# Kernel tuning notes

Measured on AMD Instinct MI355X. Metric: run time of the kernel, lower is better.

## Reference

```python
import jax, jax.numpy as jnp
import numpy as np

EPS = 1e-9


def _elementwise_ciou(b1, b2):
    # b1, b2: [..., 4] xyxy boxes. Direct O(N) CIoU (== diag of pairwise CIoU).
    x1a, y1a, x2a, y2a = b1[..., 0], b1[..., 1], b1[..., 2], b1[..., 3]
    x1b, y1b, x2b, y2b = b2[..., 0], b2[..., 1], b2[..., 2], b2[..., 3]

    iw = jnp.clip(jnp.minimum(x2a, x2b) - jnp.maximum(x1a, x1b), 0.0)
    ih = jnp.clip(jnp.minimum(y2a, y2b) - jnp.maximum(y1a, y1b), 0.0)
    inter = iw * ih
    area_a = (x2a - x1a) * (y2a - y1a)
    area_b = (x2b - x1b) * (y2b - y1b)
    union = area_a + area_b - inter
    iou = inter / (union + EPS)

    # enclosing box diagonal squared
    cw = jnp.maximum(x2a, x2b) - jnp.minimum(x1a, x1b)
    ch = jnp.maximum(y2a, y2b) - jnp.minimum(y1a, y1b)
    c2 = cw * cw + ch * ch + EPS

    # center distance squared
    dx = (x1b + x2b - x1a - x2a) * 0.5
    dy = (y1b + y2b - y1a - y2a) * 0.5
    rho2 = dx * dx + dy * dy

    # aspect-ratio consistency term
    wa, ha = x2a - x1a, y2a - y1a
    wb, hb = x2b - x1b, y2b - y1b
    v = (4.0 / (jnp.pi ** 2)) * jnp.square(
        jnp.arctan(wb / (hb + EPS)) - jnp.arctan(wa / (ha + EPS)))
    alpha = v / (1.0 - iou + v + EPS)
    return iou - rho2 / c2 - alpha * v


def _make_boxes(key, B, A):
    k1, k2 = jax.random.split(key)
    cxy = jax.random.uniform(k1, (B, A, 2), jnp.float32, 0.0, 1280.0)
    wh = jax.random.uniform(k2, (B, A, 2), jnp.float32, 4.0, 200.0)
    return jnp.concatenate([cxy - wh * 0.5, cxy + wh * 0.5], axis=-1)


def setup_inputs() -> dict:
    key = jax.random.key(0)
    B, A = 64, 33600
    k1, k2, k3, k4 = jax.random.split(key, 4)
    predicts_bbox = _make_boxes(k1, B, A)
    targets_bbox = _make_boxes(k2, B, A)
    valid_masks = jax.random.bernoulli(k3, 0.3, (B, A))
    box_norm = jax.random.uniform(k4, (B, A), jnp.float32) * valid_masks
    cls_norm = jnp.maximum(valid_masks.sum().astype(jnp.float32), 1.0)
    return {
        "predicts_bbox": predicts_bbox,
        "targets_bbox": targets_bbox,
        "valid_masks": valid_masks,
        "box_norm": box_norm,
        "cls_norm": cls_norm,
    }


def reference(predicts_bbox, targets_bbox, valid_masks, box_norm, cls_norm):
    m = valid_masks.astype(predicts_bbox.dtype)  # [B, A]
    iou = _elementwise_ciou(predicts_bbox, targets_bbox) * m
    loss_iou = ((1.0 - iou) * box_norm * m).sum() / cls_norm
    return loss_iou, iou
```

## Files before the change

kernel.cpp:

```cpp
#include <hip/hip_runtime.h>
#include <math.h>

#define EPSF 1e-9f

__global__ __launch_bounds__(256) void box_loss_kernel(
    const float4* __restrict__ pb, const float4* __restrict__ tb,
    const int*    __restrict__ mask, const float* __restrict__ bnorm,
    const float*  __restrict__ cls_norm, float* __restrict__ out, int n)
{
    const int stride = gridDim.x * blockDim.x;
    float acc = 0.0f;
    for (int i = blockIdx.x * blockDim.x + threadIdx.x; i < n; i += stride) {
        const float4 a = pb[i];
        const float4 b = tb[i];

        float iw = fminf(a.z, b.z) - fmaxf(a.x, b.x); iw = fmaxf(iw, 0.0f);
        float ih = fminf(a.w, b.w) - fmaxf(a.y, b.y); ih = fmaxf(ih, 0.0f);
        float inter = iw * ih;

        float wa = a.z - a.x, ha = a.w - a.y;
        float wb = b.z - b.x, hb = b.w - b.y;
        float uni = wa * ha + wb * hb - inter;
        float iou = inter / (uni + EPSF);

        float cw = fmaxf(a.z, b.z) - fminf(a.x, b.x);
        float ch = fmaxf(a.w, b.w) - fminf(a.y, b.y);
        float c2 = cw * cw + ch * ch + EPSF;

        float dx = (b.x + b.z - a.x - a.z) * 0.5f;
        float dy = (b.y + b.w - a.y - a.w) * 0.5f;
        float rho2 = dx * dx + dy * dy;

        float datan = atanf(wb / (hb + EPSF)) - atanf(wa / (ha + EPSF));
        const float c4pi2 = 4.0f / (float)(M_PI * M_PI);
        float v = c4pi2 * datan * datan;
        float alpha = v / (1.0f - iou + v + EPSF);

        float ciou = iou - rho2 / c2 - alpha * v;

        float m = (float)mask[i];
        float iou_m = ciou * m;
        out[1 + i] = iou_m;
        acc += (1.0f - iou_m) * bnorm[i] * m;
    }

    #pragma unroll
    for (int off = 32; off > 0; off >>= 1)
        acc += __shfl_down(acc, off, 64);

    __shared__ float lds[4];
    const int lane = threadIdx.x & 63;
    const int wid  = threadIdx.x >> 6;
    if (lane == 0) lds[wid] = acc;
    __syncthreads();
    if (threadIdx.x == 0) {
        float s = lds[0] + lds[1] + lds[2] + lds[3];
        atomicAdd(out, s / cls_norm[0]);
    }
}

extern "C" void kernel_launch(void* const* d_in, const int* in_sizes, int n_in,
                              void* d_out, int out_size, void* d_ws, size_t ws_size,
                              hipStream_t stream) {
    const float4* pb    = (const float4*)d_in[0];
    const float4* tb    = (const float4*)d_in[1];
    const int*    mask  = (const int*)  d_in[2];
    const float*  bnorm = (const float*)d_in[3];
    const float*  cls   = (const float*)d_in[4];
    float*        out   = (float*)d_out;
    const int n = in_sizes[2];

    hipMemsetAsync(d_out, 0, sizeof(float), stream);

    const int block = 256;
    const int grid  = 2048;
    box_loss_kernel<<<grid, block, 0, stream>>>(pb, tb, mask, bnorm, cls, out, n);
}
```

Baseline: 134.1 us.

## Replace atanf pair with single polynomial atan, use rcp, unroll loads

```diff
diff --git a/kernel.cpp b/kernel.cpp
--- a/kernel.cpp
+++ b/kernel.cpp
@@ -2,6 +2,55 @@
 #include <math.h>
 
 #define EPSF 1e-9f
+#define UNROLL 4
+
+__device__ __forceinline__ float fast_atan(float z) {
+    float az = fabsf(z);
+    float rz = __builtin_amdgcn_rcpf(az);
+    float t  = az > 1.0f ? rz : az;
+    float t2 = t * t;
+    float p = fmaf(t2, 0.0208351f, -0.0851330f);
+    p = fmaf(t2, p, 0.1801410f);
+    p = fmaf(t2, p, -0.3302995f);
+    p = fmaf(t2, p, 0.9998660f);
+    p = p * t;
+    float r = az > 1.0f ? 1.5707963f - p : p;
+    return z < 0.0f ? -r : r;
+}
+
+__device__ __forceinline__ float ciou_masked(float4 a, float4 b, float m,
+                                             float bn, float* acc) {
+    float iw = fminf(a.z, b.z) - fmaxf(a.x, b.x); iw = fmaxf(iw, 0.0f);
+    float ih = fminf(a.w, b.w) - fmaxf(a.y, b.y); ih = fmaxf(ih, 0.0f);
+    float inter = iw * ih;
+
+    float wa = a.z - a.x, ha = a.w - a.y;
+    float wb = b.z - b.x, hb = b.w - b.y;
+    float uni = wa * ha + wb * hb - inter;
+    float iou = inter * __builtin_amdgcn_rcpf(uni + EPSF);
+
+    float cw = fmaxf(a.z, b.z) - fminf(a.x, b.x);
+    float ch = fmaxf(a.w, b.w) - fminf(a.y, b.y);
+    float c2 = fmaf(cw, cw, fmaf(ch, ch, EPSF));
+
+    float dx = (b.x + b.z - a.x - a.z) * 0.5f;
+    float dy = (b.y + b.w - a.y - a.w) * 0.5f;
+    float rho2 = fmaf(dx, dx, dy * dy);
+
+    float hap = ha + EPSF, hbp = hb + EPSF;
+    float num = fmaf(wb, hap, -wa * hbp);
+    float den = fmaf(hap, hbp, wa * wb);
+    float datan = fast_atan(num * __builtin_amdgcn_rcpf(den));
+
+    const float c4pi2 = 0.40528473456f;
+    float v = c4pi2 * datan * datan;
+    float av = v * v * __builtin_amdgcn_rcpf(1.0f - iou + v + EPSF);
+
+    float ciou = iou - rho2 * __builtin_amdgcn_rcpf(c2) - av;
+    float iou_m = ciou * m;
+    *acc += (1.0f - iou_m) * bn * m;
+    return iou_m;
+}
 
 __global__ __launch_bounds__(256) void box_loss_kernel(
     const float4* __restrict__ pb, const float4* __restrict__ tb,
@@ -9,39 +58,25 @@
     const float*  __restrict__ cls_norm, float* __restrict__ out, int n)
 {
     const int stride = gridDim.x * blockDim.x;
+    const int tid = blockIdx.x * blockDim.x + threadIdx.x;
     float acc = 0.0f;
-    for (int i = blockIdx.x * blockDim.x + threadIdx.x; i < n; i += stride) {
-        const float4 a = pb[i];
-        const float4 b = tb[i];
 
-        float iw = fminf(a.z, b.z) - fmaxf(a.x, b.x); iw = fmaxf(iw, 0.0f);
-        float ih = fminf(a.w, b.w) - fmaxf(a.y, b.y); ih = fmaxf(ih, 0.0f);
-        float inter = iw * ih;
-
-        float wa = a.z - a.x, ha = a.w - a.y;
-        float wb = b.z - b.x, hb = b.w - b.y;
-        float uni = wa * ha + wb * hb - inter;
-        float iou = inter / (uni + EPSF);
-
-        float cw = fmaxf(a.z, b.z) - fminf(a.x, b.x);
-        float ch = fmaxf(a.w, b.w) - fminf(a.y, b.y);
-        float c2 = cw * cw + ch * ch + EPSF;
-
-        float dx = (b.x + b.z - a.x - a.z) * 0.5f;
-        float dy = (b.y + b.w - a.y - a.w) * 0.5f;
-        float rho2 = dx * dx + dy * dy;
-
-        float datan = atanf(wb / (hb + EPSF)) - atanf(wa / (ha + EPSF));
-        const float c4pi2 = 4.0f / (float)(M_PI * M_PI);
-        float v = c4pi2 * datan * datan;
-        float alpha = v / (1.0f - iou + v + EPSF);
-
-        float ciou = iou - rho2 / c2 - alpha * v;
-
-        float m = (float)mask[i];
-        float iou_m = ciou * m;
-        out[1 + i] = iou_m;
-        acc += (1.0f - iou_m) * bnorm[i] * m;
+    float4 a[UNROLL], b[UNROLL];
+    int    mk[UNROLL];
+    float  bn[UNROLL];
+    int    idx[UNROLL];
+    #pragma unroll
+    for (int u = 0; u < UNROLL; ++u) {
+        int i = tid + u * stride;
+        idx[u] = i;
+        if (i < n) { a[u] = pb[i]; b[u] = tb[i]; mk[u] = mask[i]; bn[u] = bnorm[i]; }
+        else       { mk[u] = 0; bn[u] = 0.0f;
+                     a[u] = make_float4(0,0,1,1); b[u] = make_float4(0,0,1,1); }
+    }
+    #pragma unroll
+    for (int u = 0; u < UNROLL; ++u) {
+        float r = ciou_masked(a[u], b[u], (float)mk[u], bn[u], &acc);
+        if (idx[u] < n) out[1 + idx[u]] = r;
     }
 
     #pragma unroll
@@ -73,6 +108,7 @@
     hipMemsetAsync(d_out, 0, sizeof(float), stream);
 
     const int block = 256;
-    const int grid  = 2048;
+    const int per_block = block * UNROLL;
+    const int grid = (n + per_block - 1) / per_block;
     box_loss_kernel<<<grid, block, 0, stream>>>(pb, tb, mask, bnorm, cls, out, n);
 }
```

Measured after the change: 134.0 us. Within noise of the previous version (-0.0%).
